# Performance work log

Hardware: AMD Instinct MI355X
Metric: run time of the kernel (lower is better)

The kernel has to match this reference:

```python
import jax, jax.numpy as jnp
import numpy as np

LN_EPS = 1e-5


def setup_inputs() -> dict:
    key = jax.random.key(0)
    ks = jax.random.split(key, 6)
    B, M, N, D = 16, 128, 128, 128
    NM, H = 16, 512
    xav = float(np.sqrt(2.0 / (D + D)))  # xavier_normal over (in_dim, out_dim) fan
    return {
        "x": jax.random.normal(ks[0], (B, M, N, D), jnp.float32),
        "w1": jax.random.normal(ks[1], (D, D, NM, 2), jnp.float32) * xav,
        "w2": jax.random.normal(ks[2], (D, D, NM, 2), jnp.float32) * xav,
        "ff_w0": jax.random.normal(ks[3], (D, H), jnp.float32) * float(1.0 / np.sqrt(D)),
        "ff_b0": jnp.zeros((H,), jnp.float32),
        "ff_w1": jax.random.normal(ks[4], (H, D), jnp.float32) * float(1.0 / np.sqrt(H)),
        "ff_b1": jnp.zeros((D,), jnp.float32),
        "ln_g": jnp.ones((D,), jnp.float32),
        "ln_b": jnp.zeros((D,), jnp.float32),
    }


def _layer_norm(h, g, b):
    mu = jnp.mean(h, axis=-1, keepdims=True)
    var = jnp.mean(jnp.square(h - mu), axis=-1, keepdims=True)
    return (h - mu) * jax.lax.rsqrt(var + LN_EPS) * g + b


def _forward_fourier(x, w1, w2):
    # x: [B, M, N, I] -> [B, I, M, N]
    xt = jnp.transpose(x, (0, 3, 1, 2))
    B, I, M, N = xt.shape
    nm = w1.shape[2]
    cw1 = w1[..., 0] + 1j * w1[..., 1]  # [I, O, nm]
    cw2 = w2[..., 0] + 1j * w2[..., 1]
    O = cw1.shape[1]

    # Fourier along last axis (y)
    fty = jnp.fft.rfft(xt, axis=-1, norm="ortho")                    # [B,I,M,N//2+1]
    f1 = jnp.einsum("bixy,ioy->boxy", fty[..., :nm], cw1)            # [B,O,M,nm]
    pad_y = jnp.zeros((B, O, M, N // 2 + 1 - nm), dtype=f1.dtype)
    xy = jnp.fft.irfft(jnp.concatenate([f1, pad_y], axis=-1), n=N, axis=-1, norm="ortho")

    # Fourier along second-to-last axis (x)
    ftx = jnp.fft.rfft(xt, axis=-2, norm="ortho")                    # [B,I,M//2+1,N]
    f2 = jnp.einsum("bixy,iox->boxy", ftx[:, :, :nm, :], cw2)        # [B,O,nm,N]
    pad_x = jnp.zeros((B, O, M // 2 + 1 - nm, N), dtype=f2.dtype)
    xx = jnp.fft.irfft(jnp.concatenate([f2, pad_x], axis=-2), n=M, axis=-2, norm="ortho")

    return jnp.transpose(xx + xy, (0, 2, 3, 1))  # [B,M,N,O]


def reference(x, w1, w2, ff_w0, ff_b0, ff_w1, ff_b1, ln_g, ln_b):
    h = _forward_fourier(x, w1, w2)
    # backcast FeedForward: Linear -> ReLU -> Linear -> LayerNorm (dropout=0)
    h1 = jax.nn.relu(jnp.einsum("bmni,ih->bmnh", h, ff_w0) + ff_b0)
    h2 = jnp.einsum("bmnh,ho->bmno", h1, ff_w1) + ff_b1
    return _layer_norm(h2, ln_g, ln_b)
```

## Files before the change

kernel.cpp:

```cpp
#include <hip/hip_runtime.h>


#define LN_EPS 1e-5f
#define NMODES 16
#define FROW 4096
#define HROW 16384

typedef __attribute__((ext_vector_type(8))) short short8;
typedef __attribute__((ext_vector_type(8))) ushort ushort8;
typedef __attribute__((ext_vector_type(4))) short short4v;
typedef __attribute__((ext_vector_type(4))) float f32x4;

__device__ __forceinline__ ushort f2bf(float f) {
    unsigned u = __float_as_uint(f);
    unsigned r = (u + 0x7FFFu + ((u >> 16) & 1u)) >> 16;
    return (ushort)r;
}
__device__ __forceinline__ float bf2f(ushort h) {
    return __uint_as_float(((unsigned)h) << 16);
}

__global__ void k_setup(float* __restrict__ Tc, float* __restrict__ Ts,
                        float* __restrict__ IT) {
    const float invs = 0.08838834764831845f;
    for (int idx = threadIdx.x; idx < NMODES * 128; idx += blockDim.x) {
        int k = idx >> 7, n = idx & 127;
        int p = (k * n) & 127;
        float th = (float)p * (6.283185307179586f / 128.0f);
        float c = cosf(th), s = sinf(th);
        Tc[idx] = c * invs;
        Ts[idx] = -s * invs;
        float ck = (k == 0) ? invs : 2.0f * invs;
        IT[n * 32 + 2 * k]     = ck * c;
        IT[n * 32 + 2 * k + 1] = -ck * s;
    }
}

__global__ void k_wpack(const float* __restrict__ w, ushort* __restrict__ Wph,
                        ushort* __restrict__ Wpl) {
    int idx = blockIdx.x * 256 + threadIdx.x;
    int k  = idx >> 16;
    int op = (idx >> 8) & 255;
    int ip = idx & 255;
    int i = ip & 127, o = op & 127;
    const float* base = w + (((i << 7) | o) * NMODES + k) * 2;
    float re = base[0], im = base[1];
    float v = (ip < 128) ? ((op < 128) ? re : im)
                         : ((op < 128) ? -im : re);
    ushort hi = f2bf(v);
    ushort lo = f2bf(v - bf2f(hi));
    Wph[idx] = hi;
    Wpl[idx] = lo;
}

__global__ __launch_bounds__(256) void k_wcvt(const float* __restrict__ w0,
        const float* __restrict__ w1, ushort* __restrict__ w0t,
        ushort* __restrict__ w1t) {
    int idx = blockIdx.x * 256 + threadIdx.x;
    int h = idx >> 7, k = idx & 127;
    w0t[idx] = f2bf(w0[k * 512 + h]);
    int o = idx >> 9, hh = idx & 511;
    w1t[idx] = f2bf(w1[hh * 128 + o]);
}

__global__ __launch_bounds__(128) void k_fft(const float* __restrict__ x,
        const float* __restrict__ Tc, const float* __restrict__ Ts,
        float* __restrict__ F, int mode) {
    __shared__ float Tc_s[NMODES * 128];
    __shared__ float Ts_s[NMODES * 128];
    for (int e = threadIdx.x; e < NMODES * 128; e += 128) {
        Tc_s[e] = Tc[e];
        Ts_s[e] = Ts[e];
    }
    __syncthreads();
    int row = blockIdx.x;
    int base, ts;
    if (mode == 0) { base = row * HROW; ts = 128; }
    else { base = (row >> 7) * 2097152 + (row & 127) * 128; ts = 16384; }
    int i = threadIdx.x;
    float re[NMODES], im[NMODES];
#pragma unroll
    for (int k = 0; k < NMODES; ++k) { re[k] = 0.f; im[k] = 0.f; }
    for (int tb = 0; tb < 32; ++tb) {
        int t0 = tb * 4;
        float xv0 = x[base + (t0 + 0) * ts + i];
        float xv1 = x[base + (t0 + 1) * ts + i];
        float xv2 = x[base + (t0 + 2) * ts + i];
        float xv3 = x[base + (t0 + 3) * ts + i];
#pragma unroll
        for (int k = 0; k < NMODES; ++k) {
            f32x4 c4 = *(const f32x4*)&Tc_s[k * 128 + t0];
            f32x4 s4 = *(const f32x4*)&Ts_s[k * 128 + t0];
            re[k] += xv0 * c4[0] + xv1 * c4[1] + xv2 * c4[2] + xv3 * c4[3];
            im[k] += xv0 * s4[0] + xv1 * s4[1] + xv2 * s4[2] + xv3 * s4[3];
        }
    }
    float* outp = F + row * FROW;
#pragma unroll
    for (int k = 0; k < NMODES; ++k) {
        outp[k * 256 + i]       = re[k];
        outp[k * 256 + 128 + i] = im[k];
    }
}

__global__ __launch_bounds__(256) void k_mixm(const float* __restrict__ A,
        const ushort* __restrict__ Wph, const ushort* __restrict__ Wpl,
        float* __restrict__ outF) {
    __shared__ ushort Ah[32 * 264];
    __shared__ ushort Al[32 * 264];
    int tid = threadIdx.x;
    int kt = blockIdx.x & 15;
    int bm0 = (blockIdx.x >> 4) * 32;
    {
        int row = tid >> 3, cg = tid & 7;
        const float* arow = A + (bm0 + row) * FROW + kt * 256 + cg * 32;
        ushort* ah = &Ah[row * 264 + cg * 32];
        ushort* al = &Al[row * 264 + cg * 32];
#pragma unroll
        for (int j = 0; j < 8; ++j) {
            f32x4 v = *(const f32x4*)(arow + j * 4);
            short4v h4, l4;
#pragma unroll
            for (int q = 0; q < 4; ++q) {
                ushort h = f2bf(v[q]);
                h4[q] = (short)h;
                l4[q] = (short)f2bf(v[q] - bf2f(h));
            }
            *(short4v*)(ah + j * 4) = h4;
            *(short4v*)(al + j * 4) = l4;
        }
    }
    __syncthreads();
    int lane = tid & 63, wid = tid >> 6;
    int frow = lane & 15, fk8 = (lane >> 4) * 8, fr4 = (lane >> 4) * 4;
    f32x4 acc[2][4];
#pragma unroll
    for (int a = 0; a < 2; ++a)
#pragma unroll
        for (int c = 0; c < 4; ++c) acc[a][c] = {0.f, 0.f, 0.f, 0.f};
    const ushort* wph = Wph + kt * 65536;
    const ushort* wpl = Wpl + kt * 65536;
#pragma unroll
    for (int kk = 0; kk < 8; ++kk) {
        short8 ah0 = *(const short8*)&Ah[(frow)      * 264 + kk * 32 + fk8];
        short8 ah1 = *(const short8*)&Ah[(16 + frow) * 264 + kk * 32 + fk8];
        short8 al0 = *(const short8*)&Al[(frow)      * 264 + kk * 32 + fk8];
        short8 al1 = *(const short8*)&Al[(16 + frow) * 264 + kk * 32 + fk8];
#pragma unroll
        for (int tc = 0; tc < 4; ++tc) {
            int op = wid * 64 + tc * 16 + frow;
            int base = op * 256 + kk * 32 + fk8;
            short8 wh = *(const short8*)&wph[base];
            short8 wl = *(const short8*)&wpl[base];
            acc[0][tc] = __builtin_amdgcn_mfma_f32_16x16x32_bf16(ah0, wh, acc[0][tc], 0, 0, 0);
            acc[0][tc] = __builtin_amdgcn_mfma_f32_16x16x32_bf16(ah0, wl, acc[0][tc], 0, 0, 0);
            acc[0][tc] = __builtin_amdgcn_mfma_f32_16x16x32_bf16(al0, wh, acc[0][tc], 0, 0, 0);
            acc[1][tc] = __builtin_amdgcn_mfma_f32_16x16x32_bf16(ah1, wh, acc[1][tc], 0, 0, 0);
            acc[1][tc] = __builtin_amdgcn_mfma_f32_16x16x32_bf16(ah1, wl, acc[1][tc], 0, 0, 0);
            acc[1][tc] = __builtin_amdgcn_mfma_f32_16x16x32_bf16(al1, wh, acc[1][tc], 0, 0, 0);
        }
    }
#pragma unroll
    for (int tr = 0; tr < 2; ++tr)
#pragma unroll
        for (int tc = 0; tc < 4; ++tc)
#pragma unroll
            for (int r = 0; r < 4; ++r)
                outF[(bm0 + tr * 16 + fr4 + r) * FROW + kt * 256 + wid * 64 + tc * 16 + frow]
                    = acc[tr][tc][r];
}

__global__ __launch_bounds__(256) void k_icdft(const float* __restrict__ f,
        const float* __restrict__ IT, ushort* __restrict__ obf,
        float* __restrict__ h32, const ushort* __restrict__ hyin, int mode) {
    __shared__ float IT_s[128 * 32];
    __shared__ float f_s[32 * 128];
    int row = blockIdx.x;
    for (int e = threadIdx.x; e < 4096; e += 256) {
        IT_s[e] = IT[e];
        f_s[e]  = f[row * FROW + e];
    }
    __syncthreads();
    int o = threadIdx.x & 127, nh = threadIdx.x >> 7;
    for (int nb = 0; nb < 8; ++nb) {
        int n0 = nh * 64 + nb * 8;
        float acc[8];
#pragma unroll
        for (int j = 0; j < 8; ++j) acc[j] = 0.f;
#pragma unroll
        for (int kpb = 0; kpb < 8; ++kpb) {
            int kp0 = kpb * 4;
            float f0 = f_s[kp0 * 128 + o];
            float f1v = f_s[kp0 * 128 + 128 + o];
            float f2v = f_s[kp0 * 128 + 256 + o];
            float f3v = f_s[kp0 * 128 + 384 + o];
#pragma unroll
            for (int j = 0; j < 8; ++j) {
                f32x4 it = *(const f32x4*)&IT_s[(n0 + j) * 32 + kp0];
                acc[j] += f0 * it[0] + f1v * it[1] + f2v * it[2] + f3v * it[3];
            }
        }
        if (mode == 0) {
#pragma unroll
            for (int j = 0; j < 8; ++j)
                obf[row * HROW + (n0 + j) * 128 + o] = f2bf(acc[j]);
        } else if (mode == 1) {
#pragma unroll
            for (int j = 0; j < 8; ++j)
                h32[row * HROW + (n0 + j) * 128 + o] = acc[j];
        } else if (mode == 2) {
#pragma unroll
            for (int j = 0; j < 8; ++j) {
                int ix = (row >> 7) * 2097152 + (row & 127) * 128 + o + (n0 + j) * 16384;
                obf[ix] = f2bf(bf2f(hyin[ix]) + acc[j]);
            }
        } else {
#pragma unroll
            for (int j = 0; j < 8; ++j) {
                int ix = (row >> 7) * 2097152 + (row & 127) * 128 + o + (n0 + j) * 16384;
                obf[ix] = f2bf(h32[ix] + acc[j]);
            }
        }
    }
}

__global__ __launch_bounds__(64, 2) void k_ffn(const ushort* __restrict__ hin,
        float* __restrict__ out,
        const ushort* __restrict__ w0t, const float* __restrict__ b0,
        const ushort* __restrict__ w1t, const float* __restrict__ b1,
        const float* __restrict__ g, const float* __restrict__ bb) {
    __shared__ __align__(16) char h_raw[16384];
    __shared__ __align__(16) char h1_raw[4096];
    int lane = threadIdx.x;
    int R0 = blockIdx.x * 64;

    {
        const ushort* src = hin + (size_t)R0 * 128;
#pragma unroll 4
        for (int i = 0; i < 16; ++i) {
            int e = lane + i * 64;
            int rl = e >> 4, c8 = e & 15;
            ushort8 v = *(const ushort8*)(src + rl * 128 + c8 * 8);
            *(ushort8*)(h_raw + rl * 256 + ((c8 ^ (rl & 7)) << 4)) = v;
        }
    }
    __syncthreads();

    int frow = lane & 15, qg = lane >> 4;
    int fk8 = qg * 8, fr4 = qg * 4;
    int sw7 = frow & 7;
    int sw3 = frow & 3;

    f32x4 acc2[4][8];
#pragma unroll
    for (int a = 0; a < 4; ++a)
#pragma unroll
        for (int c = 0; c < 8; ++c) acc2[a][c] = {0.f, 0.f, 0.f, 0.f};

    short8 bfr[2][4];
#pragma unroll
    for (int tc2 = 0; tc2 < 2; ++tc2)
#pragma unroll
        for (int kk = 0; kk < 4; ++kk)
            bfr[tc2][kk] = *(const short8*)&w0t[(tc2 * 16 + frow) * 128 + kk * 32 + fk8];

#pragma unroll 1
    for (int ch = 0; ch < 16; ++ch) {
        short8 b2[8];
#pragma unroll
        for (int tc = 0; tc < 8; ++tc)
            b2[tc] = *(const short8*)&w1t[(tc * 16 + frow) * 512 + ch * 32 + fk8];
        float b0v0 = b0[ch * 32 + frow];
        float b0v1 = b0[ch * 32 + 16 + frow];

#pragma unroll
        for (int g2 = 0; g2 < 2; ++g2) {
            f32x4 acc1[2][2];
#pragma unroll
            for (int a = 0; a < 2; ++a)
#pragma unroll
                for (int c = 0; c < 2; ++c) acc1[a][c] = {0.f, 0.f, 0.f, 0.f};
#pragma unroll
            for (int kk = 0; kk < 4; ++kk)
#pragma unroll
                for (int t2 = 0; t2 < 2; ++t2) {
                    int row = (g2 * 2 + t2) * 16 + frow;
                    short8 av = *(const short8*)(h_raw + row * 256
                                 + (((kk * 4 + qg) ^ sw7) << 4));
                    acc1[t2][0] = __builtin_amdgcn_mfma_f32_16x16x32_bf16(
                        av, bfr[0][kk], acc1[t2][0], 0, 0, 0);
                    acc1[t2][1] = __builtin_amdgcn_mfma_f32_16x16x32_bf16(
                        av, bfr[1][kk], acc1[t2][1], 0, 0, 0);
                }
#pragma unroll
            for (int t2 = 0; t2 < 2; ++t2)
#pragma unroll
                for (int r = 0; r < 4; ++r) {
                    int rowl = (g2 * 2 + t2) * 16 + fr4 + r;
                    *(ushort*)(h1_raw + rowl * 64 + ((frow * 2) ^ (r << 4))) =
                        f2bf(fmaxf(acc1[t2][0][r] + b0v0, 0.f));
                    *(ushort*)(h1_raw + rowl * 64 + (((16 + frow) * 2) ^ (r << 4))) =
                        f2bf(fmaxf(acc1[t2][1][r] + b0v1, 0.f));
                }
        }

        if (ch < 15) {
#pragma unroll
            for (int tc2 = 0; tc2 < 2; ++tc2)
#pragma unroll
                for (int kk = 0; kk < 4; ++kk)
                    bfr[tc2][kk] = *(const short8*)
                        &w0t[((ch + 1) * 32 + tc2 * 16 + frow) * 128 + kk * 32 + fk8];
        }

#pragma unroll
        for (int tr = 0; tr < 4; ++tr) {
            int row = tr * 16 + frow;
            short8 a2 = *(const short8*)(h1_raw + row * 64 + ((qg ^ sw3) << 4));
#pragma unroll
            for (int tc = 0; tc < 8; ++tc)
                acc2[tr][tc] = __builtin_amdgcn_mfma_f32_16x16x32_bf16(
                    a2, b2[tc], acc2[tr][tc], 0, 0, 0);
        }
    }

    float b1v[8], gv[8], bv[8];
#pragma unroll
    for (int tc = 0; tc < 8; ++tc) {
        int o = tc * 16 + frow;
        b1v[tc] = b1[o]; gv[tc] = g[o]; bv[tc] = bb[o];
    }
#pragma unroll
    for (int tr = 0; tr < 4; ++tr)
#pragma unroll
        for (int r = 0; r < 4; ++r) {
            float s = 0.f, qq = 0.f;
#pragma unroll
            for (int tc = 0; tc < 8; ++tc) {
                float v = acc2[tr][tc][r] + b1v[tc];
                acc2[tr][tc][r] = v;
                s += v; qq += v * v;
            }
            s += __shfl_xor(s, 1); qq += __shfl_xor(qq, 1);
            s += __shfl_xor(s, 2); qq += __shfl_xor(qq, 2);
            s += __shfl_xor(s, 4); qq += __shfl_xor(qq, 4);
            s += __shfl_xor(s, 8); qq += __shfl_xor(qq, 8);
            float mu = s * (1.0f / 128.0f);
            float var = qq * (1.0f / 128.0f) - mu * mu;
            float rs = rsqrtf(fmaxf(var, 0.f) + LN_EPS);
            float* orow = &out[(size_t)(R0 + tr * 16 + fr4 + r) * 128];
#pragma unroll
            for (int tc = 0; tc < 8; ++tc)
                orow[tc * 16 + frow] = (acc2[tr][tc][r] - mu) * rs * gv[tc] + bv[tc];
        }
}

extern "C" void kernel_launch(void* const* d_in, const int* in_sizes, int n_in,
                              void* d_out, int out_size, void* d_ws, size_t ws_size,
                              hipStream_t stream) {
    (void)in_sizes; (void)n_in; (void)out_size;
    const float* x   = (const float*)d_in[0];
    const float* w1  = (const float*)d_in[1];
    const float* w2  = (const float*)d_in[2];
    const float* fw0 = (const float*)d_in[3];
    const float* fb0 = (const float*)d_in[4];
    const float* fw1 = (const float*)d_in[5];
    const float* fb1 = (const float*)d_in[6];
    const float* lng = (const float*)d_in[7];
    const float* lnb = (const float*)d_in[8];
    float* out = (float*)d_out;

    char* ws = (char*)d_ws;
    float*  Tc  = (float*)(ws);
    float*  Ts  = (float*)(ws + 8192);
    float*  IT  = (float*)(ws + 16384);
    ushort* Wph = (ushort*)(ws + 32768);
    ushort* Wpl = (ushort*)(ws + 32768 + 2097152);
    ushort* w0t = (ushort*)(ws + 4227072);
    ushort* w1t = (ushort*)(ws + 4358144);
    float*  buf0 = (float*)(ws + 4489216);
    ushort* hy   = (ushort*)(ws + 38043648);
    ushort* hsum = (ushort*)(ws + 105152512);
    const size_t need_two = 172261376ull;
    int two = (ws_size >= need_two) ? 1 : 0;
    ushort* hbfs = hy;

    k_setup<<<1, 256, 0, stream>>>(Tc, Ts, IT);
    k_wcvt <<<256, 256, 0, stream>>>(fw0, fw1, w0t, w1t);

    k_wpack<<<4096, 256, 0, stream>>>(w1, Wph, Wpl);
    k_fft  <<<2048, 128, 0, stream>>>(x, Tc, Ts, buf0, 0);
    k_mixm <<<1024, 256, 0, stream>>>(buf0, Wph, Wpl, buf0);
    if (two) k_icdft<<<2048, 256, 0, stream>>>(buf0, IT, hy, out, hy, 0);
    else     k_icdft<<<2048, 256, 0, stream>>>(buf0, IT, hy, out, hy, 1);

    k_wpack<<<4096, 256, 0, stream>>>(w2, Wph, Wpl);
    k_fft  <<<2048, 128, 0, stream>>>(x, Tc, Ts, buf0, 1);
    k_mixm <<<1024, 256, 0, stream>>>(buf0, Wph, Wpl, buf0);
    if (two) k_icdft<<<2048, 256, 0, stream>>>(buf0, IT, hsum, out, hy, 2);
    else     k_icdft<<<2048, 256, 0, stream>>>(buf0, IT, hbfs, out, hy, 3);

    k_ffn<<<4096, 64, 0, stream>>>(two ? hsum : hbfs, out,
                                   w0t, fb0, w1t, fb1, lng, lnb);
}
```

Measured before the change: 549.3 us.

## Split FFN block across two waves with double-buffered hidden tile and shared LN reduction

The FFN kernel now runs two waves per 64-row block instead of one. Each wave computes half of every 32-wide hidden chunk and half of the 128 output columns. The hidden activations go into a double-buffered, padded LDS tile synchronised with a barrier per chunk, and the LayerNorm statistics are combined across waves through shared memory. This halves per-wave accumulator registers and raises occupancy, at the cost of a barrier every chunk and an extra LDS round trip for the LN sums.

```diff
diff --git a/kernel.cpp b/kernel.cpp
--- a/kernel.cpp
+++ b/kernel.cpp
@@ -224,21 +224,24 @@
     }
 }
 
-__global__ __launch_bounds__(64, 2) void k_ffn(const ushort* __restrict__ hin,
+__global__ __launch_bounds__(128, 3) void k_ffn(const ushort* __restrict__ hin,
         float* __restrict__ out,
         const ushort* __restrict__ w0t, const float* __restrict__ b0,
         const ushort* __restrict__ w1t, const float* __restrict__ b1,
         const float* __restrict__ g, const float* __restrict__ bb) {
     __shared__ __align__(16) char h_raw[16384];
-    __shared__ __align__(16) char h1_raw[4096];
-    int lane = threadIdx.x;
+    __shared__ __align__(16) char h1_raw[2][5120];
+    __shared__ float ps_s[128];
+    __shared__ float pq_s[128];
+    int tid = threadIdx.x;
+    int wave = tid >> 6, lane = tid & 63;
     int R0 = blockIdx.x * 64;
 
     {
         const ushort* src = hin + (size_t)R0 * 128;
-#pragma unroll 4
-        for (int i = 0; i < 16; ++i) {
-            int e = lane + i * 64;
+#pragma unroll
+        for (int i = 0; i < 8; ++i) {
+            int e = tid + i * 128;
             int rl = e >> 4, c8 = e & 15;
             ushort8 v = *(const ushort8*)(src + rl * 128 + c8 * 8);
             *(ushort8*)(h_raw + rl * 256 + ((c8 ^ (rl & 7)) << 4)) = v;
@@ -249,85 +252,71 @@
     int frow = lane & 15, qg = lane >> 4;
     int fk8 = qg * 8, fr4 = qg * 4;
     int sw7 = frow & 7;
-    int sw3 = frow & 3;
-
-    f32x4 acc2[4][8];
+
+    f32x4 acc2[4][4];
 #pragma unroll
     for (int a = 0; a < 4; ++a)
 #pragma unroll
-        for (int c = 0; c < 8; ++c) acc2[a][c] = {0.f, 0.f, 0.f, 0.f};
-
-    short8 bfr[2][4];
-#pragma unroll
-    for (int tc2 = 0; tc2 < 2; ++tc2)
-#pragma unroll
-        for (int kk = 0; kk < 4; ++kk)
-            bfr[tc2][kk] = *(const short8*)&w0t[(tc2 * 16 + frow) * 128 + kk * 32 + fk8];
+        for (int c = 0; c < 4; ++c) acc2[a][c] = {0.f, 0.f, 0.f, 0.f};
+
+    short8 bfr[4];
+#pragma unroll
+    for (int kk = 0; kk < 4; ++kk)
+        bfr[kk] = *(const short8*)&w0t[(wave * 16 + frow) * 128 + kk * 32 + fk8];
 
 #pragma unroll 1
     for (int ch = 0; ch < 16; ++ch) {
-        short8 b2[8];
-#pragma unroll
-        for (int tc = 0; tc < 8; ++tc)
-            b2[tc] = *(const short8*)&w1t[(tc * 16 + frow) * 512 + ch * 32 + fk8];
-        float b0v0 = b0[ch * 32 + frow];
-        float b0v1 = b0[ch * 32 + 16 + frow];
-
-#pragma unroll
-        for (int g2 = 0; g2 < 2; ++g2) {
-            f32x4 acc1[2][2];
-#pragma unroll
-            for (int a = 0; a < 2; ++a)
-#pragma unroll
-                for (int c = 0; c < 2; ++c) acc1[a][c] = {0.f, 0.f, 0.f, 0.f};
+        short8 b2[4];
+#pragma unroll
+        for (int tc = 0; tc < 4; ++tc)
+            b2[tc] = *(const short8*)&w1t[(wave * 64 + tc * 16 + frow) * 512 + ch * 32 + fk8];
+        float b0v = b0[ch * 32 + wave * 16 + frow];
+
+        f32x4 acc1[4];
+#pragma unroll
+        for (int a = 0; a < 4; ++a) acc1[a] = {0.f, 0.f, 0.f, 0.f};
+#pragma unroll
+        for (int kk = 0; kk < 4; ++kk)
+#pragma unroll
+            for (int tr = 0; tr < 4; ++tr) {
+                short8 av = *(const short8*)(h_raw + (tr * 16 + frow) * 256
+                             + (((kk * 4 + qg) ^ sw7) << 4));
+                acc1[tr] = __builtin_amdgcn_mfma_f32_16x16x32_bf16(
+                    av, bfr[kk], acc1[tr], 0, 0, 0);
+            }
+        char* h1w = h1_raw[ch & 1];
+#pragma unroll
+        for (int tr = 0; tr < 4; ++tr)
+#pragma unroll
+            for (int r = 0; r < 4; ++r)
+                *(ushort*)(h1w + (tr * 16 + fr4 + r) * 80 + wave * 32 + frow * 2) =
+                    f2bf(fmaxf(acc1[tr][r] + b0v, 0.f));
+
+        if (ch < 15) {
 #pragma unroll
             for (int kk = 0; kk < 4; ++kk)
-#pragma unroll
-                for (int t2 = 0; t2 < 2; ++t2) {
-                    int row = (g2 * 2 + t2) * 16 + frow;
-                    short8 av = *(const short8*)(h_raw + row * 256
-                                 + (((kk * 4 + qg) ^ sw7) << 4));
-                    acc1[t2][0] = __builtin_amdgcn_mfma_f32_16x16x32_bf16(
-                        av, bfr[0][kk], acc1[t2][0], 0, 0, 0);
-                    acc1[t2][1] = __builtin_amdgcn_mfma_f32_16x16x32_bf16(
-                        av, bfr[1][kk], acc1[t2][1], 0, 0, 0);
-                }
-#pragma unroll
-            for (int t2 = 0; t2 < 2; ++t2)
-#pragma unroll
-                for (int r = 0; r < 4; ++r) {
-                    int rowl = (g2 * 2 + t2) * 16 + fr4 + r;
-                    *(ushort*)(h1_raw + rowl * 64 + ((frow * 2) ^ (r << 4))) =
-                        f2bf(fmaxf(acc1[t2][0][r] + b0v0, 0.f));
-                    *(ushort*)(h1_raw + rowl * 64 + (((16 + frow) * 2) ^ (r << 4))) =
-                        f2bf(fmaxf(acc1[t2][1][r] + b0v1, 0.f));
-                }
-        }
-
-        if (ch < 15) {
-#pragma unroll
-            for (int tc2 = 0; tc2 < 2; ++tc2)
-#pragma unroll
-                for (int kk = 0; kk < 4; ++kk)
-                    bfr[tc2][kk] = *(const short8*)
-                        &w0t[((ch + 1) * 32 + tc2 * 16 + frow) * 128 + kk * 32 + fk8];
-        }
+                bfr[kk] = *(const short8*)
+                    &w0t[((ch + 1) * 32 + wave * 16 + frow) * 128 + kk * 32 + fk8];
+        }
+
+        asm volatile("s_waitcnt lgkmcnt(0)" ::: "memory");
+        __builtin_amdgcn_s_barrier();
+        asm volatile("" ::: "memory");
 
 #pragma unroll
         for (int tr = 0; tr < 4; ++tr) {
-            int row = tr * 16 + frow;
-            short8 a2 = *(const short8*)(h1_raw + row * 64 + ((qg ^ sw3) << 4));
-#pragma unroll
-            for (int tc = 0; tc < 8; ++tc)
+            short8 a2 = *(const short8*)(h1w + (tr * 16 + frow) * 80 + qg * 16);
+#pragma unroll
+            for (int tc = 0; tc < 4; ++tc)
                 acc2[tr][tc] = __builtin_amdgcn_mfma_f32_16x16x32_bf16(
                     a2, b2[tc], acc2[tr][tc], 0, 0, 0);
         }
     }
 
-    float b1v[8], gv[8], bv[8];
-#pragma unroll
-    for (int tc = 0; tc < 8; ++tc) {
-        int o = tc * 16 + frow;
+    float b1v[4], gv[4], bv[4];
+#pragma unroll
+    for (int tc = 0; tc < 4; ++tc) {
+        int o = wave * 64 + tc * 16 + frow;
         b1v[tc] = b1[o]; gv[tc] = g[o]; bv[tc] = bb[o];
     }
 #pragma unroll
@@ -336,7 +325,7 @@
         for (int r = 0; r < 4; ++r) {
             float s = 0.f, qq = 0.f;
 #pragma unroll
-            for (int tc = 0; tc < 8; ++tc) {
+            for (int tc = 0; tc < 4; ++tc) {
                 float v = acc2[tr][tc][r] + b1v[tc];
                 acc2[tr][tc][r] = v;
                 s += v; qq += v * v;
@@ -345,12 +334,26 @@
             s += __shfl_xor(s, 2); qq += __shfl_xor(qq, 2);
             s += __shfl_xor(s, 4); qq += __shfl_xor(qq, 4);
             s += __shfl_xor(s, 8); qq += __shfl_xor(qq, 8);
-            float mu = s * (1.0f / 128.0f);
-            float var = qq * (1.0f / 128.0f) - mu * mu;
+            if (frow == 0) {
+                int row = tr * 16 + fr4 + r;
+                ps_s[wave * 64 + row] = s;
+                pq_s[wave * 64 + row] = qq;
+            }
+        }
+    __syncthreads();
+#pragma unroll
+    for (int tr = 0; tr < 4; ++tr)
+#pragma unroll
+        for (int r = 0; r < 4; ++r) {
+            int row = tr * 16 + fr4 + r;
+            float S = ps_s[row] + ps_s[64 + row];
+            float Q = pq_s[row] + pq_s[64 + row];
+            float mu = S * (1.0f / 128.0f);
+            float var = Q * (1.0f / 128.0f) - mu * mu;
             float rs = rsqrtf(fmaxf(var, 0.f) + LN_EPS);
-            float* orow = &out[(size_t)(R0 + tr * 16 + fr4 + r) * 128];
-#pragma unroll
-            for (int tc = 0; tc < 8; ++tc)
+            float* orow = &out[(size_t)(R0 + row) * 128 + wave * 64];
+#pragma unroll
+            for (int tc = 0; tc < 4; ++tc)
                 orow[tc * 16 + frow] = (acc2[tr][tc][r] - mu) * rs * gv[tc] + bv[tc];
         }
 }
@@ -400,6 +403,6 @@
     if (two) k_icdft<<<2048, 256, 0, stream>>>(buf0, IT, hsum, out, hy, 2);
     else     k_icdft<<<2048, 256, 0, stream>>>(buf0, IT, hbfs, out, hy, 3);
 
-    k_ffn<<<4096, 64, 0, stream>>>(two ? hsum : hbfs, out,
-                                   w0t, fb0, w1t, fb1, lng, lnb);
-}
+    k_ffn<<<4096, 128, 0, stream>>>(two ? hsum : hbfs, out,
+                                    w0t, fb0, w1t, fb1, lng, lnb);
+}
```

New measurement: 492.5 us. 10.3% less time.
